# Optimization experiments

Hardware: AMD Instinct MI355X
Metric: run time of the kernel (lower is better)

## Reference

```python
import jax, jax.numpy as jnp
import numpy as np

B, T, K, H, KS = 4, 2048, 128, 8, 5
DIL = 2
PAD = (KS - 1) * DIL  # left causal pad = 8


def _conv1d(x, w, dil):
    # x: [b, c_in, t], w: [c_out, c_in, ks] -> [b, c_out, t_out]
    return jax.lax.conv_general_dilated(
        x, w, window_strides=(1,), padding='VALID',
        rhs_dilation=(dil,), dimension_numbers=('NCH', 'OIH', 'NCH'))


def setup_inputs() -> dict:
    key = jax.random.key(0)
    ks = jax.random.split(key, 8)
    s = 0.05
    return {
        'x': jax.random.normal(ks[0], (B, T, K), dtype=jnp.float32),
        'Wq': jax.random.normal(ks[1], (K * H, K, KS), dtype=jnp.float32) * s,
        'bq': jax.random.normal(ks[2], (K * H,), dtype=jnp.float32) * s,
        'Wk': jax.random.normal(ks[3], (K * H, K, KS), dtype=jnp.float32) * s,
        'bk': jax.random.normal(ks[4], (K * H,), dtype=jnp.float32) * s,
        'Wv': jax.random.normal(ks[5], (K * H, K, 1), dtype=jnp.float32) * s,
        'Wu': jax.random.normal(ks[6], (K, K * H), dtype=jnp.float32) * s,
        'bu': jax.random.normal(ks[7], (K,), dtype=jnp.float32) * s,
    }


def reference(x, Wq, bq, Wk, bk, Wv, Wu, bu):
    b, t, k = x.shape
    h = Wq.shape[0] // k
    silu = jax.nn.silu

    xt = jnp.transpose(x, (0, 2, 1))               # [b, k, t]
    xp = jnp.pad(xt, ((0, 0), (0, 0), (PAD, 0)))   # causal left pad

    # dilated convs -> view(b, k, h, t) (channel split: k outer, h inner, as in torch)
    q = silu(_conv1d(xp, Wq, DIL) + bq[None, :, None]).reshape(b, k, h, t)
    kk = silu(_conv1d(xp, Wk, DIL) + bk[None, :, None]).reshape(b, k, h, t)
    v = silu(_conv1d(xt, Wv, 1)).reshape(b, k, h, t)

    # -> (b, h, t, k)
    q = jnp.transpose(q, (0, 2, 3, 1))
    kk = jnp.transpose(kk, (0, 2, 3, 1))
    v = jnp.transpose(v, (0, 2, 3, 1))

    scale = k ** 0.25
    q = q / scale
    kk = kk / scale

    # faithful to torch: transpose(1,2) -> (b,t,h,k) then contiguous view (b*h, t, k)
    q2 = jnp.transpose(q, (0, 2, 1, 3)).reshape(b * h, t, k)
    k2 = jnp.transpose(kk, (0, 2, 1, 3)).reshape(b * h, t, k)
    v2 = jnp.transpose(v, (0, 2, 1, 3)).reshape(b * h, t, k)

    weights = jnp.einsum('mtd,msd->mts', q2, k2)   # [b*h, t, t]
    causal = jnp.triu(jnp.ones((t, t), dtype=bool), 1)  # mask_next, not diag
    weights = jnp.where(causal[None], -jnp.inf, weights)
    attn = jax.nn.softmax(weights, axis=2)
    out = jnp.einsum('mts,msd->mtd', attn, v2)     # [b*h, t, k]

    out = out.reshape(b, h, t, k).transpose(0, 2, 1, 3).reshape(b, t, k * h)
    return silu(out @ Wu.T + bu)
```

## Files before the change

kernel.cpp:

```cpp
#include <hip/hip_runtime.h>
#include <hip/hip_bf16.h>
#include <stdint.h>


typedef __attribute__((ext_vector_type(8))) short bf16x8;
typedef __attribute__((ext_vector_type(4))) float f32x4;
typedef __attribute__((ext_vector_type(4))) int   i32x4;
typedef unsigned short ushort_t;

__device__ __forceinline__ unsigned short f2bf(float x){
  union{float f; unsigned u;} v; v.f = x;
  unsigned r = v.u + 0x7FFFu + ((v.u >> 16) & 1u);
  return (unsigned short)(r >> 16);
}
__device__ __forceinline__ float silu_f(float x){ return x / (1.f + __expf(-x)); }

__device__ __forceinline__ int cvt_pk_bf16(float lo, float hi){
  int r;
  asm("v_cvt_pk_bf16_f32 %0, %1, %2" : "=v"(r) : "v"(lo), "v"(hi));
  return r;
}

__device__ __forceinline__ void async_cp16(void* lds, const void* g){
  __builtin_amdgcn_global_load_lds(
      (const __attribute__((address_space(1))) unsigned int*)g,
      (__attribute__((address_space(3))) unsigned int*)lds, 16, 0, 0);
}

__global__ __launch_bounds__(256) void prep(const float* __restrict__ Wq,
                                            const float* __restrict__ Wk,
                                            const float* __restrict__ Wv,
                                            const float* __restrict__ Wu,
                                            const float* __restrict__ x,
                                            ushort_t* __restrict__ W2p,
                                            ushort_t* __restrict__ Wvp,
                                            ushort_t* __restrict__ Wub,
                                            ushort_t* __restrict__ Xpad){
  int n = blockIdx.x;
  int tid = threadIdx.x;
  if (n < 2048){
    int qk = n >> 10, h = (n >> 7) & 7, d = n & 127;
    const float* src = (qk ? Wk : Wq) + (size_t)(d*8 + h)*640;
    for (int rp = tid; rp < 640; rp += 256){
      int j = rp >> 7, ci = rp & 127;
      W2p[(size_t)n*640 + rp] = f2bf(src[ci*5 + j]);
    }
  } else if (n < 3072){
    int co = n - 2048;
    for (int r = tid; r < 128; r += 256)
      Wvp[(size_t)co*128 + r] = f2bf(Wv[(size_t)co*128 + r]);
  } else if (n < 3200){
    int j = n - 3072;
    for (int r = tid; r < 1024; r += 256)
      Wub[(size_t)j*1024 + r] = f2bf(Wu[(size_t)j*1024 + r]);
  } else {
    int idx = n - 3200;
    int b   = idx & 3;
    int rt  = (idx >> 2) * 2 + (tid >> 7);
    int ci  = tid & 127;
    int t   = rt - 8;
    ushort_t v = 0;
    if (t >= 0) v = f2bf(x[((size_t)(b*2048 + t))*128 + ci]);
    Xpad[((size_t)(b*2056 + rt))*128 + ci] = v;
  }
}

__global__ __launch_bounds__(256) void gemm_qkv(
    const ushort_t* __restrict__ Xpad,
    const ushort_t* __restrict__ W2p,
    const ushort_t* __restrict__ Wvp,
    const float* __restrict__ bq, const float* __restrict__ bk,
    ushort_t* __restrict__ Q2, ushort_t* __restrict__ K2,
    ushort_t* __restrict__ V2t)
{
  __shared__ ushort_t As[2][128*32] __attribute__((aligned(16)));
  __shared__ ushort_t Bs[2][128*32] __attribute__((aligned(16)));
  int bt0 = blockIdx.y * 128;
  int tid = threadIdx.x;
  int w = tid >> 6, ln = tid & 63;
  int lc = ln & 15, lg = ln >> 4;
  int mi = (w & 1) * 64, nj = (w >> 1) * 64;
  int srow = ln >> 2;
  int kseg = (ln & 3) * 8;
  int b = bt0 >> 11, tl0 = bt0 & 2047;

  f32x4 acc[4][4];
  #pragma unroll
  for (int si = 0; si < 4; si++)
    #pragma unroll
    for (int sj = 0; sj < 4; sj++) acc[si][sj] = (f32x4){0.f,0.f,0.f,0.f};

  if (blockIdx.x < 16){
    int n0 = blockIdx.x * 128;
    const ushort_t* gA = Xpad + (size_t)(b*2056 + tl0 + w*32 + srow)*128 + kseg;
    const ushort_t* gB = W2p + (size_t)(n0  + w*32 + srow)*640 + kseg;

    auto stageAB = [&](int kk, int bsel){
      int j = kk >> 2, ci0 = (kk & 3) * 32;
      int r0 = kk * 32;
      const ushort_t* a0 = gA + (size_t)(2*j)*128 + ci0;
      async_cp16(&As[bsel][w*1024],       a0);
      async_cp16(&As[bsel][w*1024 + 512], a0 + 16*128);
      async_cp16(&Bs[bsel][w*1024],       gB + r0);
      async_cp16(&Bs[bsel][w*1024 + 512], gB + r0 + 16*640);
    };

    stageAB(0, 0);
    for (int kk = 0; kk < 20; kk++){
      int bsel = kk & 1;
      if (kk + 1 < 20){
        stageAB(kk + 1, bsel ^ 1);
        asm volatile("s_waitcnt vmcnt(4)\n\ts_barrier" ::: "memory");
      } else {
        asm volatile("s_waitcnt vmcnt(0)\n\ts_barrier" ::: "memory");
      }
      bf16x8 af[4], bfr[4];
      #pragma unroll
      for (int si = 0; si < 4; si++)
        af[si] = *(const bf16x8*)&As[bsel][(mi + 16*si + lc)*32 + 8*lg];
      #pragma unroll
      for (int sj = 0; sj < 4; sj++)
        bfr[sj] = *(const bf16x8*)&Bs[bsel][(nj + 16*sj + lc)*32 + 8*lg];
      #pragma unroll
      for (int si = 0; si < 4; si++)
        #pragma unroll
        for (int sj = 0; sj < 4; sj++)
          acc[si][sj] = __builtin_amdgcn_mfma_f32_16x16x32_bf16(af[si], bfr[sj],
                                                                acc[si][sj], 0,0,0);
      asm volatile("s_barrier" ::: "memory");
    }

    const float inv_scale = 0.29730177875068026f;
    int qk = n0 >> 10, h = (n0 >> 7) & 7;
    const float* bias = qk ? bk : bq;
    ushort_t* dst = qk ? K2 : Q2;
    float bv[4];
    #pragma unroll
    for (int sj = 0; sj < 4; sj++) bv[sj] = bias[(nj + 16*sj + lc)*8 + h];

    #pragma unroll
    for (int si = 0; si < 4; si++){
      int btb = bt0 + mi + 16*si + 4*lg;
      #pragma unroll
      for (int r = 0; r < 4; r++){
        int t = btb + r;
        int bb = t >> 11, tl = t & 2047;
        size_t rowoff = ((size_t)(bb*8 + (tl >> 8))*2048 + (tl & 255)*8 + h)*128;
        #pragma unroll
        for (int sj = 0; sj < 4; sj++){
          int d = nj + 16*sj + lc;
          dst[rowoff + d] = f2bf(silu_f(acc[si][sj][r] + bv[sj]) * inv_scale);
        }
      }
    }
  } else {
    int n0 = (blockIdx.x - 16) * 128;
    const ushort_t* gA = Xpad + (size_t)(b*2056 + 8 + tl0 + w*32 + srow)*128 + kseg;
    const ushort_t* gB = Wvp  + (size_t)(n0 + w*32 + srow)*128 + kseg;

    for (int kk = 0; kk < 4; kk++){
      int r0 = kk * 32;
      __syncthreads();
      async_cp16(&As[0][w*1024],        gA + r0);
      async_cp16(&As[0][w*1024 + 512],  gA + r0 + 16*128);
      async_cp16(&Bs[0][w*1024],        gB + r0);
      async_cp16(&Bs[0][w*1024 + 512],  gB + r0 + 16*128);
      __syncthreads();
      bf16x8 af[4], bfr[4];
      #pragma unroll
      for (int si = 0; si < 4; si++)
        af[si] = *(const bf16x8*)&As[0][(mi + 16*si + lc)*32 + 8*lg];
      #pragma unroll
      for (int sj = 0; sj < 4; sj++)
        bfr[sj] = *(const bf16x8*)&Bs[0][(nj + 16*sj + lc)*32 + 8*lg];
      #pragma unroll
      for (int si = 0; si < 4; si++)
        #pragma unroll
        for (int sj = 0; sj < 4; sj++)
          acc[si][sj] = __builtin_amdgcn_mfma_f32_16x16x32_bf16(af[si], bfr[sj],
                                                                acc[si][sj], 0,0,0);
    }

    #pragma unroll
    for (int si = 0; si < 4; si++){
      int btb = bt0 + mi + 16*si + 4*lg;
      #pragma unroll
      for (int r = 0; r < 4; r++){
        int t = btb + r;
        int bb = t >> 11, tl = t & 2047;
        int mm = bb*8 + (tl >> 8);
        int tpb = (tl & 255)*8;
        #pragma unroll
        for (int sj = 0; sj < 4; sj++){
          int co = n0 + nj + 16*sj + lc;
          int d = co >> 3, hh = co & 7;
          V2t[((size_t)mm*128 + d)*2048 + tpb + hh] = f2bf(silu_f(acc[si][sj][r]));
        }
      }
    }
  }
}

__global__ __launch_bounds__(256) void attn(
    const ushort_t* __restrict__ Q2,
    const ushort_t* __restrict__ K2,
    const ushort_t* __restrict__ V2t,
    ushort_t* __restrict__ O2)
{
  __shared__ i32x4 kbuf[2][1024];
  __shared__ i32x4 vbuf[2][1024];

  int bid = blockIdx.x;
  int m   = ((bid & 7) << 2) | ((bid >> 3) & 3);
  int ip  = bid >> 5;
  int tid = threadIdx.x;
  int w = tid >> 6, l = tid & 63;
  int lc = l & 15, lg = l >> 4;

  int iA = 31 - ip, iB = ip;
  int ntA = iA + 1;
  const int nt = 33;

  const size_t mQ = (size_t)m * 2048;
  const ushort_t* Kbase = K2  + mQ * 128;
  const ushort_t* Vbase = V2t + (size_t)m * 128 * 2048;
  int hb = m & 7, bI = m >> 3;

  int psel[4];
  #pragma unroll
  for (int w2 = 0; w2 < 4; w2++)
    psel[w2] = ((((2*(lg & 1) + (w2 >> 1)) << 4) | lc) << 2);

  auto stage = [&](int s0, int bsel){
    const ushort_t* krow = Kbase + (size_t)(s0 + w*16 + lc)*128 + 8*lg;
    #pragma unroll
    for (int c = 0; c < 4; c++)
      async_cp16(&kbuf[bsel][(w*4 + c)*64], krow + 32*c);
    #pragma unroll
    for (int j = 0; j < 4; j++){
      int dt = w*2 + (j >> 1);
      const ushort_t* vrow = Vbase + (size_t)(dt*16 + lc)*2048
                             + s0 + (j & 1)*32 + 8*lg;
      async_cp16(&vbuf[bsel][(w*4 + j)*64], vrow);
    }
  };

  int qb = iA*64 + w*16;
  bf16x8 qfrag[4];
  {
    const ushort_t* qp = Q2 + (mQ + qb + lc)*128 + 8*lg;
    #pragma unroll
    for (int c = 0; c < 4; c++) qfrag[c] = *(const bf16x8*)(qp + 32*c);
  }
  f32x4 oacc[8];
  #pragma unroll
  for (int dt = 0; dt < 8; dt++) oacc[dt] = (f32x4){0.f,0.f,0.f,0.f};
  float lrow = 0.f;

  const float LOG2E = 1.4426950408889634f;
  const float EOFF  = -11.541560327111707f;

  stage(0, 0);

  for (int step = 0; step < nt; step++){
    if (step == ntA){
      float lt = lrow;
      lt += __shfl_xor(lt, 16);
      lt += __shfl_xor(lt, 32);
      float invl = 1.f / lt;
      size_t obase = ((size_t)(bI*2048 + qb + lc))*1024 + hb*128 + 4*lg;
      #pragma unroll
      for (int dt = 0; dt < 8; dt++){
        uint2 val;
        val.x = (unsigned)cvt_pk_bf16(oacc[dt][0]*invl, oacc[dt][1]*invl);
        val.y = (unsigned)cvt_pk_bf16(oacc[dt][2]*invl, oacc[dt][3]*invl);
        *(uint2*)&O2[obase + 16*dt] = val;
      }
      qb = iB*64 + w*16;
      const ushort_t* qp = Q2 + (mQ + qb + lc)*128 + 8*lg;
      #pragma unroll
      for (int c = 0; c < 4; c++) qfrag[c] = *(const bf16x8*)(qp + 32*c);
      #pragma unroll
      for (int dt = 0; dt < 8; dt++) oacc[dt] = (f32x4){0.f,0.f,0.f,0.f};
      lrow = 0.f;
    }
    int local = (step < ntA) ? step : step - ntA;
    bool isLast = (step == ntA - 1) || (step == nt - 1);
    int s0 = local * 64;
    int bsel = step & 1;

    if (step + 1 < nt){
      int nl = (step + 1 < ntA) ? step + 1 : step + 1 - ntA;
      stage(nl*64, bsel ^ 1);
      asm volatile("s_waitcnt vmcnt(8)\n\ts_barrier" ::: "memory");
    } else {
      asm volatile("s_waitcnt vmcnt(0)\n\ts_barrier" ::: "memory");
    }

    f32x4 sacc[4];
    #pragma unroll
    for (int st = 0; st < 4; st++){
      f32x4 a2 = (f32x4){0.f,0.f,0.f,0.f};
      #pragma unroll
      for (int c = 0; c < 4; c++){
        bf16x8 kf = *(bf16x8*)&kbuf[bsel][(st*4 + c)*64 + l];
        a2 = __builtin_amdgcn_mfma_f32_16x16x32_bf16(kf, qfrag[c], a2, 0, 0, 0);
      }
      sacc[st] = a2;
    }
    if (isLast){
      int qg = qb + lc;
      #pragma unroll
      for (int st = 0; st < 4; st++)
        #pragma unroll
        for (int r = 0; r < 4; r++){
          int sg = s0 + st*16 + 4*lg + r;
          if (sg > qg) sacc[st][r] = -1e30f;
        }
    }

    float p_[4][4];
    #pragma unroll
    for (int st = 0; st < 4; st++)
      #pragma unroll
      for (int r = 0; r < 4; r++){
        float sv = fminf(fmaf(sacc[st][r], LOG2E, EOFF), 108.f);
        float pv = __builtin_amdgcn_exp2f(sv);
        p_[st][r] = pv;
        lrow += pv;
      }

    #pragma unroll
    for (int ks = 0; ks < 2; ks++){
      int pk0[2], pk1[2];
      #pragma unroll
      for (int pa = 0; pa < 2; pa++){
        pk0[pa] = cvt_pk_bf16(p_[2*ks][2*pa],   p_[2*ks][2*pa+1]);
        pk1[pa] = cvt_pk_bf16(p_[2*ks+1][2*pa], p_[2*ks+1][2*pa+1]);
      }
      union { int i[4]; bf16x8 v; } bfr;
      #pragma unroll
      for (int w2 = 0; w2 < 4; w2++){
        int v0 = __builtin_amdgcn_ds_bpermute(psel[w2], pk0[w2 & 1]);
        int v1 = __builtin_amdgcn_ds_bpermute(psel[w2], pk1[w2 & 1]);
        bfr.i[w2] = (lg >> 1) ? v1 : v0;
      }
      #pragma unroll
      for (int dt = 0; dt < 8; dt++){
        bf16x8 vf = *(bf16x8*)&vbuf[bsel][(dt*2 + ks)*64 + l];
        oacc[dt] = __builtin_amdgcn_mfma_f32_16x16x32_bf16(vf, bfr.v, oacc[dt], 0, 0, 0);
      }
    }
    asm volatile("s_barrier" ::: "memory");
  }

  float lt = lrow;
  lt += __shfl_xor(lt, 16);
  lt += __shfl_xor(lt, 32);
  float invl = 1.f / lt;
  size_t obase = ((size_t)(bI*2048 + qb + lc))*1024 + hb*128 + 4*lg;
  #pragma unroll
  for (int dt = 0; dt < 8; dt++){
    uint2 val;
    val.x = (unsigned)cvt_pk_bf16(oacc[dt][0]*invl, oacc[dt][1]*invl);
    val.y = (unsigned)cvt_pk_bf16(oacc[dt][2]*invl, oacc[dt][3]*invl);
    *(uint2*)&O2[obase + 16*dt] = val;
  }
}

__global__ __launch_bounds__(256) void finalmm(
    const ushort_t* __restrict__ O2,
    const ushort_t* __restrict__ Wub,
    const float* __restrict__ bu,
    float* __restrict__ out)
{
  __shared__ ushort_t As[32*32]  __attribute__((aligned(16)));
  __shared__ ushort_t Bs[128*32] __attribute__((aligned(16)));
  int bt0 = blockIdx.x * 32;
  int tid = threadIdx.x;
  int w = tid >> 6, ln = tid & 63;
  int lc = ln & 15, lg = ln >> 4;
  int nj = w * 32;
  int srow = ln >> 2;
  int kseg = (ln & 3) * 8;

  f32x4 acc[2][2];
  #pragma unroll
  for (int si = 0; si < 2; si++)
    #pragma unroll
    for (int sj = 0; sj < 2; sj++) acc[si][sj] = (f32x4){0.f,0.f,0.f,0.f};

  const ushort_t* gA = O2  + (size_t)(bt0 + (w & 1)*16 + srow)*1024 + kseg;
  const ushort_t* gB = Wub + (size_t)(w*32 + srow)*1024 + kseg;

  for (int kk = 0; kk < 32; kk++){
    int r0 = kk * 32;
    __syncthreads();
    if (w < 2) async_cp16(&As[w*512], gA + r0);
    async_cp16(&Bs[w*1024],       gB + r0);
    async_cp16(&Bs[w*1024 + 512], gB + r0 + 16*1024);
    __syncthreads();
    bf16x8 af[2], bfr[2];
    #pragma unroll
    for (int si = 0; si < 2; si++)
      af[si] = *(const bf16x8*)&As[(16*si + lc)*32 + 8*lg];
    #pragma unroll
    for (int sj = 0; sj < 2; sj++)
      bfr[sj] = *(const bf16x8*)&Bs[(nj + 16*sj + lc)*32 + 8*lg];
    #pragma unroll
    for (int si = 0; si < 2; si++)
      #pragma unroll
      for (int sj = 0; sj < 2; sj++)
        acc[si][sj] = __builtin_amdgcn_mfma_f32_16x16x32_bf16(af[si], bfr[sj],
                                                              acc[si][sj], 0,0,0);
  }

  float bv[2];
  #pragma unroll
  for (int sj = 0; sj < 2; sj++) bv[sj] = bu[nj + 16*sj + lc];
  #pragma unroll
  for (int si = 0; si < 2; si++)
    #pragma unroll
    for (int r = 0; r < 4; r++){
      int t = bt0 + 16*si + 4*lg + r;
      #pragma unroll
      for (int sj = 0; sj < 2; sj++)
        out[(size_t)t*128 + nj + 16*sj + lc] = silu_f(acc[si][sj][r] + bv[sj]);
    }
}

extern "C" void kernel_launch(void* const* d_in, const int* in_sizes, int n_in,
                              void* d_out, int out_size, void* d_ws, size_t ws_size,
                              hipStream_t stream) {
  const float* x  = (const float*)d_in[0];
  const float* Wq = (const float*)d_in[1];
  const float* bq = (const float*)d_in[2];
  const float* Wk = (const float*)d_in[3];
  const float* bk = (const float*)d_in[4];
  const float* Wv = (const float*)d_in[5];
  const float* Wu = (const float*)d_in[6];
  const float* bu = (const float*)d_in[7];
  float* out = (float*)d_out;

  char* ws = (char*)d_ws;
  ushort_t* Q2   = (ushort_t*)(ws + 0);
  ushort_t* K2   = (ushort_t*)(ws + 16777216);
  ushort_t* V2t  = (ushort_t*)(ws + 33554432);
  ushort_t* O2   = (ushort_t*)(ws + 50331648);
  ushort_t* Xpad = (ushort_t*)(ws + 67108864);
  ushort_t* W2p  = (ushort_t*)(ws + 70254592);
  ushort_t* Wvp  = (ushort_t*)(ws + 73400320);
  ushort_t* Wub  = (ushort_t*)(ws + 74448896);

  prep<<<dim3(7312, 1, 1), 256, 0, stream>>>(Wq, Wk, Wv, Wu, x,
                                             W2p, Wvp, Wub, Xpad);

  gemm_qkv<<<dim3(24, 64, 1), 256, 0, stream>>>(Xpad, W2p, Wvp, bq, bk,
                                                Q2, K2, V2t);

  attn<<<dim3(512, 1, 1), 256, 0, stream>>>(Q2, K2, V2t, O2);
  finalmm<<<dim3(256, 1, 1), 256, 0, stream>>>(O2, Wub, bu, out);
}
```

Measured before the change: 206.5 us.

## Double-buffer LDS staging in V-projection and final projection GEMM loops

The V-projection branch of the conv kernel and the final output-projection kernel now double-buffer their shared-memory tiles. Each loop issues async global-to-LDS copies for the next k-slice before computing on the current one. Hand-written s_waitcnt vmcnt and s_barrier sequences replace the paired __syncthreads, so load latency can overlap the MFMA work. The cost is twice the LDS footprint in finalmm and reliance on exact outstanding-load counts, which differ between waves that issue three copies and waves that issue two.

```diff
diff --git a/kernel.cpp b/kernel.cpp
--- a/kernel.cpp
+++ b/kernel.cpp
@@ -158,27 +158,37 @@
     const ushort_t* gA = Xpad + (size_t)(b*2056 + 8 + tl0 + w*32 + srow)*128 + kseg;
     const ushort_t* gB = Wvp  + (size_t)(n0 + w*32 + srow)*128 + kseg;
 
+    auto stageV = [&](int kk, int bsel){
+      int r0 = kk * 32;
+      async_cp16(&As[bsel][w*1024],       gA + r0);
+      async_cp16(&As[bsel][w*1024 + 512], gA + r0 + 16*128);
+      async_cp16(&Bs[bsel][w*1024],       gB + r0);
+      async_cp16(&Bs[bsel][w*1024 + 512], gB + r0 + 16*128);
+    };
+
+    stageV(0, 0);
     for (int kk = 0; kk < 4; kk++){
-      int r0 = kk * 32;
-      __syncthreads();
-      async_cp16(&As[0][w*1024],        gA + r0);
-      async_cp16(&As[0][w*1024 + 512],  gA + r0 + 16*128);
-      async_cp16(&Bs[0][w*1024],        gB + r0);
-      async_cp16(&Bs[0][w*1024 + 512],  gB + r0 + 16*128);
-      __syncthreads();
+      int bsel = kk & 1;
+      if (kk + 1 < 4){
+        stageV(kk + 1, bsel ^ 1);
+        asm volatile("s_waitcnt vmcnt(4)\n\ts_barrier" ::: "memory");
+      } else {
+        asm volatile("s_waitcnt vmcnt(0)\n\ts_barrier" ::: "memory");
+      }
       bf16x8 af[4], bfr[4];
       #pragma unroll
       for (int si = 0; si < 4; si++)
-        af[si] = *(const bf16x8*)&As[0][(mi + 16*si + lc)*32 + 8*lg];
+        af[si] = *(const bf16x8*)&As[bsel][(mi + 16*si + lc)*32 + 8*lg];
       #pragma unroll
       for (int sj = 0; sj < 4; sj++)
-        bfr[sj] = *(const bf16x8*)&Bs[0][(nj + 16*sj + lc)*32 + 8*lg];
+        bfr[sj] = *(const bf16x8*)&Bs[bsel][(nj + 16*sj + lc)*32 + 8*lg];
       #pragma unroll
       for (int si = 0; si < 4; si++)
         #pragma unroll
         for (int sj = 0; sj < 4; sj++)
           acc[si][sj] = __builtin_amdgcn_mfma_f32_16x16x32_bf16(af[si], bfr[sj],
                                                                 acc[si][sj], 0,0,0);
+      asm volatile("s_barrier" ::: "memory");
     }
 
     #pragma unroll
@@ -374,8 +384,8 @@
     const float* __restrict__ bu,
     float* __restrict__ out)
 {
-  __shared__ ushort_t As[32*32]  __attribute__((aligned(16)));
-  __shared__ ushort_t Bs[128*32] __attribute__((aligned(16)));
+  __shared__ ushort_t As[2][32*32]  __attribute__((aligned(16)));
+  __shared__ ushort_t Bs[2][128*32] __attribute__((aligned(16)));
   int bt0 = blockIdx.x * 32;
   int tid = threadIdx.x;
   int w = tid >> 6, ln = tid & 63;
@@ -393,26 +403,36 @@
   const ushort_t* gA = O2  + (size_t)(bt0 + (w & 1)*16 + srow)*1024 + kseg;
   const ushort_t* gB = Wub + (size_t)(w*32 + srow)*1024 + kseg;
 
+  auto stageF = [&](int kk, int bsel){
+    int r0 = kk * 32;
+    if (w < 2) async_cp16(&As[bsel][w*512], gA + r0);
+    async_cp16(&Bs[bsel][w*1024],       gB + r0);
+    async_cp16(&Bs[bsel][w*1024 + 512], gB + r0 + 16*1024);
+  };
+
+  stageF(0, 0);
   for (int kk = 0; kk < 32; kk++){
-    int r0 = kk * 32;
-    __syncthreads();
-    if (w < 2) async_cp16(&As[w*512], gA + r0);
-    async_cp16(&Bs[w*1024],       gB + r0);
-    async_cp16(&Bs[w*1024 + 512], gB + r0 + 16*1024);
-    __syncthreads();
+    int bsel = kk & 1;
+    if (kk + 1 < 32){
+      stageF(kk + 1, bsel ^ 1);
+      asm volatile("s_waitcnt vmcnt(2)\n\ts_barrier" ::: "memory");
+    } else {
+      asm volatile("s_waitcnt vmcnt(0)\n\ts_barrier" ::: "memory");
+    }
     bf16x8 af[2], bfr[2];
     #pragma unroll
     for (int si = 0; si < 2; si++)
-      af[si] = *(const bf16x8*)&As[(16*si + lc)*32 + 8*lg];
+      af[si] = *(const bf16x8*)&As[bsel][(16*si + lc)*32 + 8*lg];
     #pragma unroll
     for (int sj = 0; sj < 2; sj++)
-      bfr[sj] = *(const bf16x8*)&Bs[(nj + 16*sj + lc)*32 + 8*lg];
+      bfr[sj] = *(const bf16x8*)&Bs[bsel][(nj + 16*sj + lc)*32 + 8*lg];
     #pragma unroll
     for (int si = 0; si < 2; si++)
       #pragma unroll
       for (int sj = 0; sj < 2; sj++)
         acc[si][sj] = __builtin_amdgcn_mfma_f32_16x16x32_bf16(af[si], bfr[sj],
                                                               acc[si][sj], 0,0,0);
+    asm volatile("s_barrier" ::: "memory");
   }
 
   float bv[2];
```

New measurement: 203.9 us. Within noise of the previous version (-1.3%).
